# Kernel tuning notes

Measured on AMD Instinct MI355X. Metric: run time of the kernel, lower is better.

The kernel has to match this reference:

```python
import jax, jax.numpy as jnp
import numpy as np

B, D_IN, D_OUT = 8192, 512, 1024
N_PATHS, N_STEPS = 256, 50  # n_paths = min(output_size, 256); n_steps fixed at 50
T_HORIZON, DECAY_RATE = 1.0, 0.1


def setup_inputs() -> dict:
    key = jax.random.key(0)
    k_x, k_wfb, k_wagg, k_noise = jax.random.split(key, 4)
    x = jax.random.normal(k_x, (B, D_IN), dtype=jnp.float32)
    W_fb = jax.random.normal(k_wfb, (1, D_IN), dtype=jnp.float32) / np.sqrt(D_IN)
    b_fb = jnp.zeros((1,), dtype=jnp.float32)
    W_agg = jax.random.normal(k_wagg, (D_OUT, N_PATHS), dtype=jnp.float32) / np.sqrt(N_PATHS)
    b_agg = jnp.zeros((D_OUT,), dtype=jnp.float32)
    # Pre-drawn standard normal increments for all batch items / paths / steps
    noise = jax.random.normal(k_noise, (B, N_PATHS, N_STEPS), dtype=jnp.float32)
    return {"x": x, "W_fb": W_fb, "b_fb": b_fb, "W_agg": W_agg, "b_agg": b_agg, "noise": noise}


def reference(x, W_fb, b_fb, W_agg, b_agg, noise):
    # feedback_transform + sigmoid -> scalar feedback per sample  [B]
    feedback = jax.nn.sigmoid(x @ W_fb.T + b_fb)[:, 0]
    # original extracts feedback via .item(): no grad flows into the simulation
    fb = jax.lax.stop_gradient(feedback)

    dt = jnp.asarray(T_HORIZON / N_STEPS, dtype=x.dtype)
    t = jnp.arange(N_STEPS, dtype=x.dtype) * dt                 # [S]
    # per-sample, per-step drift-free diffusion scale: 0.5 + fb * exp(-decay * t)
    scale = 0.5 + fb[:, None] * jnp.exp(-DECAY_RATE * t)[None, :]  # [B, S]

    # endpoint of X_{t+1} = X_t + sqrt(dt) * scale_t * noise_t, X_0 = 0
    # == sqrt(dt) * sum_t scale[b,t] * noise[b,p,t]
    endpoints = jnp.einsum('bps,bs->bp', noise, scale) * jnp.sqrt(dt)  # [B, P]

    # path_aggregator linear
    return endpoints @ W_agg.T + b_agg  # [B, D_OUT]
```

## Files before the change

kernel.cpp:

```cpp
#include <hip/hip_runtime.h>
#include <math.h>


#define B_TOTAL 8192
#define D_IN    512
#define D_OUT   1024
#define NP      256
#define NS      50
#define BT      16
#define THREADS 256
#define PCHUNK  8
#define NCHUNK  (NP / PCHUNK)
#define CHUNK_F4 1600
#define ROW_F4   100
#define EP_STRIDE 264

#define SQRT_DT 0.14142135623730951f

typedef __bf16 bf16x8 __attribute__((ext_vector_type(8)));
typedef float  f32x4  __attribute__((ext_vector_type(4)));

__device__ __forceinline__ unsigned short f2bf(float f) {
    unsigned u = __float_as_uint(f);
    return (unsigned short)((u + 0x7FFFu + ((u >> 16) & 1u)) >> 16);
}

__global__ __launch_bounds__(THREADS, 2) void bicep_main(
    const float* __restrict__ x,
    const float* __restrict__ Wfb,
    const float* __restrict__ bfb,
    const float* __restrict__ Wagg,
    const float* __restrict__ bagg,
    const float* __restrict__ noise,
    float* __restrict__ out)
{
    __shared__ __align__(16) float nbuf[2][CHUNK_F4 * 4];
    __shared__ __align__(16) unsigned short ep_bf[BT * EP_STRIDE];
    __shared__ float fb_s[BT];
    __shared__ float bagg_s[D_OUT];

    const int tid  = threadIdx.x;
    const int lane = tid & 63;
    const int wave = tid >> 6;
    const int b0   = blockIdx.x * BT;

    {
        #pragma unroll
        for (int i = 0; i < D_OUT / THREADS; ++i)
            bagg_s[i * THREADS + tid] = bagg[i * THREADS + tid];

        const float bf_b = bfb[0];
        const float4* wf = (const float4*)Wfb + lane * 2;
        float4 wa = wf[0], wb = wf[1];
        #pragma unroll
        for (int rr = 0; rr < 4; ++rr) {
            int row = wave * 4 + rr;
            const float4* xr = (const float4*)(x + (size_t)(b0 + row) * D_IN) + lane * 2;
            float4 xa = xr[0], xb = xr[1];
            float p = xa.x*wa.x + xa.y*wa.y + xa.z*wa.z + xa.w*wa.w
                    + xb.x*wb.x + xb.y*wb.y + xb.z*wb.z + xb.w*wb.w;
            #pragma unroll
            for (int mm = 32; mm >= 1; mm >>= 1) p += __shfl_xor(p, mm, 64);
            if (lane == 0) fb_s[row] = 1.0f / (1.0f + __expf(-(p + bf_b)));
        }
    }

    const int h     = tid & 1;
    const int jpair = tid >> 1;
    const int c_row = jpair >> 3;
    const int c_pl  = jpair & 7;

    float ereg[25];
    #pragma unroll
    for (int s = 0; s < 25; ++s)
        ereg[s] = __expf(-0.002f * (float)(h * 25 + s));

    const float4* nptr[7];
    #pragma unroll
    for (int r = 0; r < 7; ++r) {
        int g4  = r * 256 + tid;
        int row = g4 / 100;
        int off = g4 - row * 100;
        if (row > BT - 1) row = BT - 1;
        nptr[r] = (const float4*)(noise + (size_t)(b0 + row) * (NP * NS)) + off;
    }

    float4 v[7];
    v[6] = make_float4(0.f, 0.f, 0.f, 0.f);
    #pragma unroll
    for (int r = 0; r < 6; ++r) v[r] = nptr[r][0];
    if (tid < 64) v[6] = nptr[6][0];

    for (int c = 0; c < NCHUNK; ++c) {
        float* nb = nbuf[c & 1];
        #pragma unroll
        for (int r = 0; r < 6; ++r) ((float4*)nb)[r * 256 + tid] = v[r];
        if (tid < 64) ((float4*)nb)[6 * 256 + tid] = v[6];

        if (c + 1 < NCHUNK) {
            #pragma unroll
            for (int r = 0; r < 6; ++r) v[r] = nptr[r][(c + 1) * ROW_F4];
            if (tid < 64) v[6] = nptr[6][(c + 1) * ROW_F4];
        }

        __syncthreads();

        const float* src = &nb[c_row * (PCHUNK * NS) + c_pl * NS + h * 25];
        float s0 = 0.f, s1 = 0.f;
        #pragma unroll
        for (int s = 0; s < 25; ++s) {
            float nv = src[s];
            s0 += nv;
            s1 = fmaf(ereg[s], nv, s1);
        }
        s0 += __shfl_xor(s0, 1, 64);
        s1 += __shfl_xor(s1, 1, 64);
        if (h == 0) {
            float ep = SQRT_DT * fmaf(fb_s[c_row], s1, 0.5f * s0);
            ep_bf[c_row * EP_STRIDE + c * PCHUNK + c_pl] = f2bf(ep);
        }
    }
    __syncthreads();

    {
        const int m  = lane & 15;
        const int kg = lane >> 4;

        bf16x8 afr[8];
        #pragma unroll
        for (int ks = 0; ks < 8; ++ks)
            afr[ks] = *(const bf16x8*)&ep_bf[m * EP_STRIDE + ks * 32 + kg * 8];

        #pragma unroll 2
        for (int i = 0; i < 16; ++i) {
            int O = wave * 16 + i;
            const float* wp = Wagg + (size_t)(O * 16 + m) * NP + kg * 8;
            f32x4 acc = {0.f, 0.f, 0.f, 0.f};
            #pragma unroll
            for (int ks = 0; ks < 8; ++ks) {
                float4 wa = *(const float4*)(wp + ks * 32);
                float4 wb = *(const float4*)(wp + ks * 32 + 4);
                bf16x8 bfr = { (__bf16)wa.x, (__bf16)wa.y, (__bf16)wa.z, (__bf16)wa.w,
                               (__bf16)wb.x, (__bf16)wb.y, (__bf16)wb.z, (__bf16)wb.w };
                acc = __builtin_amdgcn_mfma_f32_16x16x32_bf16(afr[ks], bfr, acc, 0, 0, 0);
            }
            float bias = bagg_s[O * 16 + m];
            #pragma unroll
            for (int r = 0; r < 4; ++r)
                out[(size_t)(b0 + kg * 4 + r) * D_OUT + O * 16 + m] = acc[r] + bias;
        }
    }
}

extern "C" void kernel_launch(void* const* d_in, const int* in_sizes, int n_in,
                              void* d_out, int out_size, void* d_ws, size_t ws_size,
                              hipStream_t stream) {
    const float* x     = (const float*)d_in[0];
    const float* Wfb   = (const float*)d_in[1];
    const float* bfb   = (const float*)d_in[2];
    const float* Wagg  = (const float*)d_in[3];
    const float* bagg  = (const float*)d_in[4];
    const float* noise = (const float*)d_in[5];
    float* out = (float*)d_out;
    (void)d_ws; (void)ws_size;

    bicep_main<<<dim3(B_TOTAL / BT), dim3(THREADS), 0, stream>>>(
        x, Wfb, bfb, Wagg, bagg, noise, out);
}
```

Baseline: 667.8 us.

## Stream noise chunks directly into LDS with async global_load_lds double buffering

Replaces the register-staged noise prefetch, which loaded into VGPRs and then stored to LDS, with direct global-to-LDS async copies into the alternate buffer. Explicit vmcnt waits and raw barriers order the double-buffered chunks. The goal is to free the VGPRs and store instructions used for staging and keep more loads in flight. In exchange the LDS buffer is padded so every thread issues a 7th copy (redundant clamped loads), and a second barrier is added per chunk.

```diff
diff --git a/kernel.cpp b/kernel.cpp
--- a/kernel.cpp
+++ b/kernel.cpp
@@ -12,6 +12,7 @@
 #define PCHUNK  8
 #define NCHUNK  (NP / PCHUNK)
 #define CHUNK_F4 1600
+#define CHUNK_F4P 1792
 #define ROW_F4   100
 #define EP_STRIDE 264
 
@@ -25,6 +26,13 @@
     return (unsigned short)((u + 0x7FFFu + ((u >> 16) & 1u)) >> 16);
 }
 
+__device__ __forceinline__ void async_cp16(const float4* g, float* l) {
+    __builtin_amdgcn_global_load_lds(
+        (const __attribute__((address_space(1))) void*)g,
+        (__attribute__((address_space(3))) void*)l,
+        16, 0, 0);
+}
+
 __global__ __launch_bounds__(THREADS, 2) void bicep_main(
     const float* __restrict__ x,
     const float* __restrict__ Wfb,
@@ -34,7 +42,7 @@
     const float* __restrict__ noise,
     float* __restrict__ out)
 {
-    __shared__ __align__(16) float nbuf[2][CHUNK_F4 * 4];
+    __shared__ __align__(16) float nbuf[2][CHUNK_F4P * 4];
     __shared__ __align__(16) unsigned short ep_bf[BT * EP_STRIDE];
     __shared__ float fb_s[BT];
     __shared__ float bagg_s[D_OUT];
@@ -81,29 +89,30 @@
         int g4  = r * 256 + tid;
         int row = g4 / 100;
         int off = g4 - row * 100;
-        if (row > BT - 1) row = BT - 1;
+        if (row > BT - 1) { row = BT - 1; off = 0; }
         nptr[r] = (const float4*)(noise + (size_t)(b0 + row) * (NP * NS)) + off;
     }
 
-    float4 v[7];
-    v[6] = make_float4(0.f, 0.f, 0.f, 0.f);
+    __syncthreads();
+
     #pragma unroll
-    for (int r = 0; r < 6; ++r) v[r] = nptr[r][0];
-    if (tid < 64) v[6] = nptr[6][0];
+    for (int r = 0; r < 7; ++r)
+        async_cp16(nptr[r], nbuf[0] + (r * 256 + wave * 64) * 4);
 
     for (int c = 0; c < NCHUNK; ++c) {
-        float* nb = nbuf[c & 1];
-        #pragma unroll
-        for (int r = 0; r < 6; ++r) ((float4*)nb)[r * 256 + tid] = v[r];
-        if (tid < 64) ((float4*)nb)[6 * 256 + tid] = v[6];
+        const float* nb = nbuf[c & 1];
 
         if (c + 1 < NCHUNK) {
+            float* nbn = nbuf[(c + 1) & 1];
             #pragma unroll
-            for (int r = 0; r < 6; ++r) v[r] = nptr[r][(c + 1) * ROW_F4];
-            if (tid < 64) v[6] = nptr[6][(c + 1) * ROW_F4];
+            for (int r = 0; r < 7; ++r)
+                async_cp16(nptr[r] + (c + 1) * ROW_F4, nbn + (r * 256 + wave * 64) * 4);
+            asm volatile("s_waitcnt vmcnt(7)" ::: "memory");
+        } else {
+            asm volatile("s_waitcnt vmcnt(0)" ::: "memory");
         }
-
-        __syncthreads();
+        __builtin_amdgcn_s_barrier();
+        asm volatile("" ::: "memory");
 
         const float* src = &nb[c_row * (PCHUNK * NS) + c_pl * NS + h * 25];
         float s0 = 0.f, s1 = 0.f;
@@ -119,6 +128,9 @@
             float ep = SQRT_DT * fmaf(fb_s[c_row], s1, 0.5f * s0);
             ep_bf[c_row * EP_STRIDE + c * PCHUNK + c_pl] = f2bf(ep);
         }
+
+        asm volatile("" ::: "memory");
+        __builtin_amdgcn_s_barrier();
     }
     __syncthreads();
 
```

Measured after the change: 618.7 us. -7.4%, faster.
